# Kernel tuning notes

Measured on AMD Instinct MI355X. Metric: run time of the kernel, lower is better.

The kernel has to match this reference:

```python
import jax, jax.numpy as jnp
import numpy as np
from jax import lax


def _lstm_seq(x, W, U, b):
    """Keras-style LSTM over full sequence. x: [B,T,D] -> hs: [B,T,H].
    Gate order i, f, c(g), o; zero initial state; sigmoid/tanh activations."""
    B, T, D = x.shape
    H = U.shape[0]
    # Precompute input projection for all timesteps (one big GEMM).
    xz = jnp.einsum('btd,dg->btg', x, W) + b  # [B,T,4H]

    def step(carry, xz_t):
        h, c = carry
        z = xz_t + h @ U  # [B,4H]
        i, f, g, o = jnp.split(z, 4, axis=-1)
        i = jax.nn.sigmoid(i)
        f = jax.nn.sigmoid(f)
        g = jnp.tanh(g)
        o = jax.nn.sigmoid(o)
        c = f * c + i * g
        h = o * jnp.tanh(c)
        return (h, c), h

    h0 = jnp.zeros((B, H), dtype=x.dtype)
    c0 = jnp.zeros((B, H), dtype=x.dtype)
    (_, _), hs = lax.scan(step, (h0, c0), jnp.swapaxes(xz, 0, 1))  # hs: [T,B,H]
    return jnp.swapaxes(hs, 0, 1)  # [B,T,H]


def setup_inputs() -> dict:
    key = jax.random.key(0)
    ks = jax.random.split(key, 7)
    B, T, D, H = 64, 256, 1024, 1024
    s = 0.05  # weight scale to keep gates out of saturation
    x = jax.random.normal(ks[0], (B, T, 1, D), dtype=jnp.float32)
    Wf = jax.random.normal(ks[1], (D, 4 * H), dtype=jnp.float32) * s
    Uf = jax.random.normal(ks[2], (H, 4 * H), dtype=jnp.float32) * s
    bf = jnp.zeros((4 * H,), dtype=jnp.float32)
    Wb = jax.random.normal(ks[3], (D, 4 * H), dtype=jnp.float32) * s
    Ub = jax.random.normal(ks[4], (H, 4 * H), dtype=jnp.float32) * s
    bb = jnp.zeros((4 * H,), dtype=jnp.float32)
    return {"x": x, "Wf": Wf, "Uf": Uf, "bf": bf, "Wb": Wb, "Ub": Ub, "bb": bb}


def reference(x, Wf, Uf, bf, Wb, Ub, bb):
    # call(): squeeze axis=2, BiLSTM (concat), flatten. training=False -> dropout off.
    xs = jnp.squeeze(x, axis=2)  # [B,T,D]
    h_fwd = _lstm_seq(xs, Wf, Uf, bf)  # [B,T,H]
    # go_backwards=True: process reversed sequence; Bidirectional re-reverses output.
    h_bwd = _lstm_seq(xs[:, ::-1, :], Wb, Ub, bb)[:, ::-1, :]  # [B,T,H]
    out = jnp.concatenate([h_fwd, h_bwd], axis=-1)  # [B,T,2H]
    B = out.shape[0]
    return out.reshape(B, -1)  # Flatten -> [B, T*2H]
```

## Files before the change

### kernel.cpp

```cpp
#include <hip/hip_runtime.h>
#include <hip/hip_bf16.h>

typedef unsigned short u16;
typedef unsigned long long u64;
typedef short short8 __attribute__((ext_vector_type(8)));
typedef float floatx4 __attribute__((ext_vector_type(4)));

#define BATCH 64
#define SEQT  256
#define DDIM  1024
#define HDIM  1024
#define GDIM  4096
#define MROWS 16384

__device__ __forceinline__ u16 f2bf(float f) {
  unsigned u = __builtin_bit_cast(unsigned, f);
  u += 0x7fffu + ((u >> 16) & 1u);
  return (u16)(u >> 16);
}
__device__ __forceinline__ float bf2f(u16 v) {
  unsigned u = ((unsigned)v) << 16;
  return __builtin_bit_cast(float, u);
}
__device__ __forceinline__ float xz2f(float v) { return v; }
__device__ __forceinline__ float xz2f(u16 v) { return bf2f(v); }

template <typename T> __device__ __forceinline__ T f2xz(float v);
template <> __device__ __forceinline__ float f2xz<float>(float v) { return v; }
template <> __device__ __forceinline__ u16 f2xz<u16>(float v) { return f2bf(v); }

__device__ __forceinline__ float sigm(float x) { return 1.0f / (1.0f + __expf(-x)); }
__device__ __forceinline__ float tanh_(float x) {
  float a = __expf(2.0f * fabsf(x));
  float r = 1.0f - 2.0f / (a + 1.0f);
  return x >= 0.0f ? r : -r;
}

__device__ __forceinline__ void async16(const void* g, void* l) {
  __builtin_amdgcn_global_load_lds(
      (const __attribute__((address_space(1))) unsigned int*)g,
      (__attribute__((address_space(3))) unsigned int*)l, 16, 0, 0);
}

__device__ __forceinline__ void st_agent(unsigned* p, unsigned v) {
  __hip_atomic_store(p, v, __ATOMIC_RELAXED, __HIP_MEMORY_SCOPE_AGENT);
}

__device__ __forceinline__ void grid_barrier(unsigned* arrv, int wd, int l, unsigned epoch) {
  __syncthreads();
  if (threadIdx.x == 0)
    __hip_atomic_store(arrv + wd, epoch, __ATOMIC_RELAXED, __HIP_MEMORY_SCOPE_AGENT);
  if (threadIdx.x < 64) {
    unsigned a, b;
    do {
      __builtin_amdgcn_s_sleep(2);
      a = __hip_atomic_load(arrv + l,      __ATOMIC_RELAXED, __HIP_MEMORY_SCOPE_AGENT);
      b = __hip_atomic_load(arrv + 64 + l, __ATOMIC_RELAXED, __HIP_MEMORY_SCOPE_AGENT);
    } while (!__all(a >= epoch && b >= epoch));
  }
  __syncthreads();
}

__global__ __launch_bounds__(256) void k_cvt_x(const float* __restrict__ in,
                                               u16* __restrict__ out) {
  long i = ((long)blockIdx.x * 256 + threadIdx.x) * 4;
  float4 v = *(const float4*)(in + i);
  u16 o0 = f2bf(v.x), o1 = f2bf(v.y), o2 = f2bf(v.z), o3 = f2bf(v.w);
  unsigned lo = (unsigned)o0 | ((unsigned)o1 << 16);
  unsigned hi = (unsigned)o2 | ((unsigned)o3 << 16);
  uint2 p; p.x = lo; p.y = hi;
  *(uint2*)(out + i) = p;
}

__global__ __launch_bounds__(256) void k_tc(const float* __restrict__ S0, const float* __restrict__ S1,
                                            const float* __restrict__ S2, const float* __restrict__ S3,
                                            u16* __restrict__ D0, u16* __restrict__ D1,
                                            u16* __restrict__ D2, u16* __restrict__ D3) {
  const float* src; u16* dst;
  switch (blockIdx.z) {
    case 0: src = S0; dst = D0; break;
    case 1: src = S1; dst = D1; break;
    case 2: src = S2; dst = D2; break;
    default: src = S3; dst = D3; break;
  }
  __shared__ __align__(16) float tl[64][65];
  const int k0 = blockIdx.x * 64, n0 = blockIdx.y * 64;
  const int tid = threadIdx.x, col = tid & 63, rq = tid >> 6;
#pragma unroll
  for (int i = 0; i < 16; i++) {
    int r = i * 4 + rq;
    tl[r][col] = src[(long)(k0 + r) * GDIM + n0 + col];
  }
  __syncthreads();
#pragma unroll
  for (int i = 0; i < 16; i++) {
    int r = i * 4 + rq;
    dst[(long)(n0 + r) * DDIM + k0 + col] = f2bf(tl[col][r]);
  }
}

template <typename XZT>
__global__ __launch_bounds__(256) void k_gemm(const u16* __restrict__ A,
                                              const u16* __restrict__ BtF, const u16* __restrict__ BtB,
                                              const float* __restrict__ biasF, const float* __restrict__ biasB,
                                              XZT* __restrict__ xzF, XZT* __restrict__ xzB) {
  const u16* Bt = blockIdx.z ? BtB : BtF;
  const float* bias = blockIdx.z ? biasB : biasF;
  XZT* xz = blockIdx.z ? xzB : xzF;
  const int m0 = blockIdx.x * 128, n0 = blockIdx.y * 128;
  __shared__ __align__(16) u16 Al[128 * 32];
  __shared__ __align__(16) u16 Bl[128 * 32];
  const int tid = threadIdx.x, w = tid >> 6, l = tid & 63;
  const int wm = w & 1, wn = w >> 1;
  floatx4 acc[4][4];
#pragma unroll
  for (int i = 0; i < 4; i++)
#pragma unroll
    for (int j = 0; j < 4; j++) acc[i][j] = (floatx4)(0.0f);

  const int srow = w * 32 + (l >> 2);
  const char* Ag = (const char*)(A + (long)(m0 + srow) * DDIM) + (l & 3) * 16;
  const char* Bg = (const char*)(Bt + (long)(n0 + srow) * DDIM) + (l & 3) * 16;
  char* Asl = (char*)Al + w * 2048;
  char* Bsl = (char*)Bl + w * 2048;

  for (int kt = 0; kt < 32; kt++) {
    __syncthreads();
    async16(Ag, Asl);
    async16(Ag + 16 * 2048, Asl + 1024);
    async16(Bg, Bsl);
    async16(Bg + 16 * 2048, Bsl + 1024);
    Ag += 64; Bg += 64;
    __syncthreads();
    short8 af[4], bfr[4];
#pragma unroll
    for (int i = 0; i < 4; i++) {
      af[i]  = *(const short8*)(Al + (wm * 64 + i * 16 + (l & 15)) * 32 + (l >> 4) * 8);
      bfr[i] = *(const short8*)(Bl + (wn * 64 + i * 16 + (l & 15)) * 32 + (l >> 4) * 8);
    }
#pragma unroll
    for (int i = 0; i < 4; i++)
#pragma unroll
      for (int j = 0; j < 4; j++)
        acc[i][j] = __builtin_amdgcn_mfma_f32_16x16x32_bf16(af[i], bfr[j], acc[i][j], 0, 0, 0);
  }
  const int c = l & 15, q = l >> 4;
#pragma unroll
  for (int j = 0; j < 4; j++) {
    const int n = n0 + wn * 64 + j * 16 + c;
    const float bv = bias[n];
#pragma unroll
    for (int i = 0; i < 4; i++) {
      const long mb = (long)(m0 + wm * 64 + i * 16 + q * 4);
#pragma unroll
      for (int r = 0; r < 4; r++)
        xz[(mb + r) * GDIM + n] = f2xz<XZT>(acc[i][j][r] + bv);
    }
  }
}

template <typename XZT>
__global__ __launch_bounds__(256, 1) void k_lstm(const XZT* __restrict__ xzF, const XZT* __restrict__ xzB,
                                                 const u16* __restrict__ UtF, const u16* __restrict__ UtB,
                                                 u16* __restrict__ hbuf, float* __restrict__ out,
                                                 unsigned* __restrict__ bar) {
  const int wg = blockIdx.x;
  const int dir = wg >> 7;
  const int wd = wg & 127;
  const int j0 = wd * 8;
  const int tid = threadIdx.x;
  const int wave = tid >> 6, l = tid & 63;
  const int c = l & 15, q = l >> 4;
  const u16* Ut = dir ? UtB : UtF;
  const XZT* xz = dir ? xzB : xzF;
  unsigned* arrv = bar + dir * 128;
  u16* hb = hbuf + (long)dir * (2 * BATCH * HDIM);

  __shared__ __align__(16) u16 U1[16 * 1032];
  __shared__ float zl[64][33];

#pragma unroll
  for (int u8 = 0; u8 < 8; u8++) {
    int unit = u8 * 256 + tid;
    int r = unit >> 7, kc = unit & 127;
    int zr = (r < 8) ? (2048 + j0 + r) : (3072 + j0 + (r - 8));
    short8 v = *(const short8*)(Ut + (long)zr * DDIM + kc * 8);
    *(short8*)(&U1[r * 1032 + kc * 8]) = v;
  }
  const int zr0 = (c < 8) ? (j0 + c) : (1024 + j0 + (c - 8));
  const int zr1 = zr0 + 2048;
  short8 bU0[32];
#pragma unroll
  for (int kt = 0; kt < 32; kt++)
    bU0[kt] = *(const short8*)(Ut + (long)zr0 * DDIM + kt * 32 + q * 8);

  const int eb = tid >> 2;
  const int jj = (tid & 3) * 2;
  st_agent((unsigned*)(hb + eb * HDIM + j0 + jj), 0u);
  float cs0 = 0.0f, cs1 = 0.0f;

  const unsigned hvoff = (unsigned)(((wave * 16 + c) * HDIM + q * 8) * 2);

  float xv0[4], xv1[4];
  auto prefetch = [&](int s) {
    const int t = dir ? (SEQT - 1 - s) : s;
#pragma unroll
    for (int r = 0; r < 4; r++) {
      const long row = ((long)(wave * 16 + q * 4 + r) * SEQT + t) * GDIM;
      xv0[r] = xz2f(xz[row + zr0]);
      xv1[r] = xz2f(xz[row + zr1]);
    }
  };
  prefetch(0);

  for (int s = 0; s < SEQT; s++) {
    grid_barrier(arrv, wd, l, (unsigned)(s + 1));
    const int p = s & 1;
    const int t = dir ? (SEQT - 1 - s) : s;

    const u64 sbase = (u64)(hb + (long)p * (BATCH * HDIM));
    short8 hv[32];
#pragma unroll
    for (int kt = 0; kt < 32; kt++)
      asm volatile("global_load_dwordx4 %0, %1, %2 offset:%3 sc0 sc1"
                   : "=v"(hv[kt])
                   : "v"(hvoff), "s"(sbase), "n"(kt * 64));

    floatx4 a0 = (floatx4)(0.0f), a1 = (floatx4)(0.0f);
#pragma unroll
    for (int kt = 0; kt < 32; kt++) {
      asm volatile("s_waitcnt vmcnt(%1)" : "+v"(hv[kt]) : "n"(31 - kt));
      short8 b1 = *(const short8*)(&U1[c * 1032 + kt * 32 + q * 8]);
      a0 = __builtin_amdgcn_mfma_f32_16x16x32_bf16(hv[kt], bU0[kt], a0, 0, 0, 0);
      a1 = __builtin_amdgcn_mfma_f32_16x16x32_bf16(hv[kt], b1, a1, 0, 0, 0);
    }
#pragma unroll
    for (int r = 0; r < 4; r++) {
      const int m = wave * 16 + q * 4 + r;
      zl[m][c]      = a0[r] + xv0[r];
      zl[m][16 + c] = a1[r] + xv1[r];
    }
    __syncthreads();

    float zi0 = zl[eb][jj],      zi1 = zl[eb][jj + 1];
    float zf0 = zl[eb][8 + jj],  zf1 = zl[eb][8 + jj + 1];
    float zg0 = zl[eb][16 + jj], zg1 = zl[eb][16 + jj + 1];
    float zo0 = zl[eb][24 + jj], zo1 = zl[eb][24 + jj + 1];
    float i0 = sigm(zi0), f0 = sigm(zf0), g0 = tanh_(zg0), o0 = sigm(zo0);
    float i1 = sigm(zi1), f1 = sigm(zf1), g1 = tanh_(zg1), o1 = sigm(zo1);
    cs0 = f0 * cs0 + i0 * g0;
    cs1 = f1 * cs1 + i1 * g1;
    float h0v = o0 * tanh_(cs0), h1v = o1 * tanh_(cs1);

    unsigned hpair = (unsigned)f2bf(h0v) | ((unsigned)f2bf(h1v) << 16);
    st_agent((unsigned*)(hb + (long)(1 - p) * (BATCH * HDIM) + eb * HDIM + j0 + jj), hpair);
    float2 op = make_float2(h0v, h1v);
    *(float2*)(out + (long)eb * (SEQT * 2 * HDIM) + (long)t * (2 * HDIM) + dir * HDIM + j0 + jj) = op;

    if (s + 1 < SEQT) prefetch(s + 1);
  }
}

extern "C" void kernel_launch(void* const* d_in, const int* in_sizes, int n_in,
                              void* d_out, int out_size, void* d_ws, size_t ws_size,
                              hipStream_t stream) {
  const float* x   = (const float*)d_in[0];
  const float* Wf  = (const float*)d_in[1];
  const float* Uf  = (const float*)d_in[2];
  const float* bf_ = (const float*)d_in[3];
  const float* Wb  = (const float*)d_in[4];
  const float* Ub  = (const float*)d_in[5];
  const float* bb  = (const float*)d_in[6];
  float* out = (float*)d_out;
  char* ws = (char*)d_ws;

  const size_t SZ_XBF = (size_t)MROWS * DDIM * 2;
  const size_t SZ_WT  = (size_t)GDIM * DDIM * 2;
  const size_t SZ_H   = (size_t)2 * 2 * BATCH * HDIM * 2;

  size_t off = 2048;
  u16* xbf = (u16*)(ws + off); off += SZ_XBF;
  u16* WtF = (u16*)(ws + off); off += SZ_WT;
  u16* WtB = (u16*)(ws + off); off += SZ_WT;
  u16* UtF = (u16*)(ws + off); off += SZ_WT;
  u16* UtB = (u16*)(ws + off); off += SZ_WT;
  u16* hb  = (u16*)(ws + off); off += SZ_H;
  size_t xz_off = (off + 1023) & ~(size_t)1023;

  const size_t XZ_F32 = (size_t)MROWS * GDIM * 4;
  const size_t XZ_BF  = (size_t)MROWS * GDIM * 2;
  const bool fp32xz = ws_size >= xz_off + 2 * XZ_F32;

  unsigned* bar = (unsigned*)ws;
  hipMemsetAsync(bar, 0, 2048, stream);
  k_cvt_x<<<MROWS * DDIM / 1024, 256, 0, stream>>>(x, xbf);
  k_tc<<<dim3(16, 64, 4), 256, 0, stream>>>(Wf, Uf, Wb, Ub, WtF, UtF, WtB, UtB);

  if (fp32xz) {
    float* xzF = (float*)(ws + xz_off);
    float* xzB = (float*)(ws + xz_off + XZ_F32);
    k_gemm<float><<<dim3(128, 32, 2), 256, 0, stream>>>(xbf, WtF, WtB, bf_, bb, xzF, xzB);
    k_lstm<float><<<256, 256, 0, stream>>>(xzF, xzB, UtF, UtB, hb, out, bar);
  } else {
    u16* xzF = (u16*)(ws + xz_off);
    u16* xzB = (u16*)(ws + xz_off + XZ_BF);
    k_gemm<u16><<<dim3(128, 32, 2), 256, 0, stream>>>(xbf, WtF, WtB, bf_, bb, xzF, xzB);
    k_lstm<u16><<<256, 256, 0, stream>>>(xzF, xzB, UtF, UtB, hb, out, bar);
  }
}
```

Before: 3.535 ms.

## Mirror hidden state into per-XCD buffers so reads hit local L2

Each workgroup reads its XCD id from a hardware register and counts the workgroups per XCD and direction. Up to four leaders per group copy the shared h buffer each step into a per-XCD mirror and signal a flag. All workgroups then read h from the mirror with cached loads instead of system-coherent sc0 sc1 loads. The aim is to cut cross-XCD coherent traffic on the 64x1024 hidden state read every timestep, at the cost of an extra copy, an extra flag wait per step, and cache invalidations.

Result: no change. 3.604 ms (+1.9%).

```diff
diff --git a/kernel.cpp b/kernel.cpp
--- a/kernel.cpp
+++ b/kernel.cpp
@@ -12,6 +12,7 @@
 #define HDIM  1024
 #define GDIM  4096
 #define MROWS 16384
+#define NXCD  8
 
 __device__ __forceinline__ u16 f2bf(float f) {
   unsigned u = __builtin_bit_cast(unsigned, f);
@@ -44,6 +45,9 @@
 
 __device__ __forceinline__ void st_agent(unsigned* p, unsigned v) {
   __hip_atomic_store(p, v, __ATOMIC_RELAXED, __HIP_MEMORY_SCOPE_AGENT);
+}
+__device__ __forceinline__ unsigned ld_agent(const unsigned* p) {
+  return __hip_atomic_load(p, __ATOMIC_RELAXED, __HIP_MEMORY_SCOPE_AGENT);
 }
 
 __device__ __forceinline__ void grid_barrier(unsigned* arrv, int wd, int l, unsigned epoch) {
@@ -162,7 +166,8 @@
 template <typename XZT>
 __global__ __launch_bounds__(256, 1) void k_lstm(const XZT* __restrict__ xzF, const XZT* __restrict__ xzB,
                                                  const u16* __restrict__ UtF, const u16* __restrict__ UtB,
-                                                 u16* __restrict__ hbuf, float* __restrict__ out,
+                                                 u16* __restrict__ hbuf, u16* __restrict__ mirror,
+                                                 float* __restrict__ out,
                                                  unsigned* __restrict__ bar) {
   const int wg = blockIdx.x;
   const int dir = wg >> 7;
@@ -173,11 +178,26 @@
   const int c = l & 15, q = l >> 4;
   const u16* Ut = dir ? UtB : UtF;
   const XZT* xz = dir ? xzB : xzF;
-  unsigned* arrv = bar + dir * 128;
+  unsigned* arrv  = bar + dir * 128;
+  unsigned* flags = bar + 256;
+  unsigned* cnti  = bar + 512;
+  unsigned* cany  = bar + 768;
   u16* hb = hbuf + (long)dir * (2 * BATCH * HDIM);
 
   __shared__ __align__(16) u16 U1[16 * 1032];
   __shared__ float zl[64][33];
+  __shared__ unsigned s_xcd, s_old, s_nl, s_use;
+
+  if (tid == 0) {
+    unsigned xcc;
+    asm volatile("s_getreg_b32 %0, hwreg(20, 0, 32)" : "=s"(xcc));
+    xcc &= 7;
+    s_xcd = xcc;
+    const unsigned g = xcc * 2 + (unsigned)dir;
+    s_old = atomicAdd(&cnti[g], 1u);
+    if (s_old == 0)
+      *(volatile unsigned*)&cany[g * 32] = 0xC0FFEE00u | g;
+  }
 
 #pragma unroll
   for (int u8 = 0; u8 < 8; u8++) {
@@ -194,12 +214,20 @@
   for (int kt = 0; kt < 32; kt++)
     bU0[kt] = *(const short8*)(Ut + (long)zr0 * DDIM + kt * 32 + q * 8);
 
+  __syncthreads();
+  const unsigned myx = s_xcd;
+  const unsigned lidx = s_old;
+  const unsigned grp = myx * 2 + (unsigned)dir;
+  u16* mirb = mirror + (size_t)grp * (BATCH * HDIM);
+  unsigned* flg = flags + grp * 16;
+
   const int eb = tid >> 2;
   const int jj = (tid & 3) * 2;
   st_agent((unsigned*)(hb + eb * HDIM + j0 + jj), 0u);
   float cs0 = 0.0f, cs1 = 0.0f;
 
   const unsigned hvoff = (unsigned)(((wave * 16 + c) * HDIM + q * 8) * 2);
+  const unsigned cpoff = (unsigned)(wave * 8192 + l * 16);
 
   float xv0[4], xv1[4];
   auto prefetch = [&](int s) {
@@ -213,18 +241,64 @@
   };
   prefetch(0);
 
+  unsigned nl = 4, use_mir = 0;
   for (int s = 0; s < SEQT; s++) {
     grid_barrier(arrv, wd, l, (unsigned)(s + 1));
+    if (s == 0) {
+      asm volatile("buffer_inv sc0" ::: "memory");
+      if (tid == 0) {
+        unsigned gsz = ld_agent(&cnti[grp]);
+        s_nl = gsz < 4 ? gsz : 4;
+        s_use = (*(volatile unsigned*)&cany[grp * 32] == (0xC0FFEE00u | grp)) ? 1u : 0u;
+      }
+      __syncthreads();
+      nl = s_nl; use_mir = s_use;
+    }
     const int p = s & 1;
     const int t = dir ? (SEQT - 1 - s) : s;
-
     const u64 sbase = (u64)(hb + (long)p * (BATCH * HDIM));
+    const u64 mbase = (u64)mirb;
+
+    if (lidx < 4) {
+      for (unsigned ch = lidx; ch < 4; ch += nl) {
+        const unsigned cb = ch * 32768u + cpoff;
+        short8 cv[8];
+#pragma unroll
+        for (int i = 0; i < 8; i++)
+          asm volatile("global_load_dwordx4 %0, %1, %2 sc0 sc1"
+                       : "=v"(cv[i]) : "v"(cb + i * 1024u), "s"(sbase));
+#pragma unroll
+        for (int i = 0; i < 8; i++) {
+          asm volatile("s_waitcnt vmcnt(7)" : "+v"(cv[i]));
+          asm volatile("global_store_dwordx4 %0, %1, %2"
+                       :: "v"(cb + i * 1024u), "v"(cv[i]), "s"(mbase));
+        }
+      }
+      asm volatile("s_waitcnt vmcnt(0)" ::: "memory");
+      __syncthreads();
+      if (tid == 0) atomicAdd(flg, 1u);
+    }
+
     short8 hv[32];
-#pragma unroll
-    for (int kt = 0; kt < 32; kt++)
-      asm volatile("global_load_dwordx4 %0, %1, %2 offset:%3 sc0 sc1"
-                   : "=v"(hv[kt])
-                   : "v"(hvoff), "s"(sbase), "n"(kt * 64));
+    if (use_mir) {
+      if (tid == 0) {
+        const unsigned target = nl * (unsigned)(s + 1);
+        while (ld_agent(flg) < target) __builtin_amdgcn_s_sleep(1);
+      }
+      __syncthreads();
+      asm volatile("buffer_inv sc0" ::: "memory");
+#pragma unroll
+      for (int kt = 0; kt < 32; kt++)
+        asm volatile("global_load_dwordx4 %0, %1, %2 offset:%3"
+                     : "=v"(hv[kt])
+                     : "v"(hvoff), "s"(mbase), "n"(kt * 64));
+    } else {
+#pragma unroll
+      for (int kt = 0; kt < 32; kt++)
+        asm volatile("global_load_dwordx4 %0, %1, %2 offset:%3 sc0 sc1"
+                     : "=v"(hv[kt])
+                     : "v"(hvoff), "s"(sbase), "n"(kt * 64));
+    }
 
     floatx4 a0 = (floatx4)(0.0f), a1 = (floatx4)(0.0f);
 #pragma unroll
@@ -277,14 +351,16 @@
   const size_t SZ_XBF = (size_t)MROWS * DDIM * 2;
   const size_t SZ_WT  = (size_t)GDIM * DDIM * 2;
   const size_t SZ_H   = (size_t)2 * 2 * BATCH * HDIM * 2;
-
-  size_t off = 2048;
+  const size_t SZ_MIR = (size_t)NXCD * 2 * BATCH * HDIM * 2;
+
+  size_t off = 8192;
   u16* xbf = (u16*)(ws + off); off += SZ_XBF;
   u16* WtF = (u16*)(ws + off); off += SZ_WT;
   u16* WtB = (u16*)(ws + off); off += SZ_WT;
   u16* UtF = (u16*)(ws + off); off += SZ_WT;
   u16* UtB = (u16*)(ws + off); off += SZ_WT;
   u16* hb  = (u16*)(ws + off); off += SZ_H;
+  u16* mir = (u16*)(ws + off); off += SZ_MIR;
   size_t xz_off = (off + 1023) & ~(size_t)1023;
 
   const size_t XZ_F32 = (size_t)MROWS * GDIM * 4;
@@ -292,7 +368,7 @@
   const bool fp32xz = ws_size >= xz_off + 2 * XZ_F32;
 
   unsigned* bar = (unsigned*)ws;
-  hipMemsetAsync(bar, 0, 2048, stream);
+  hipMemsetAsync(bar, 0, 8192, stream);
   k_cvt_x<<<MROWS * DDIM / 1024, 256, 0, stream>>>(x, xbf);
   k_tc<<<dim3(16, 64, 4), 256, 0, stream>>>(Wf, Uf, Wb, Ub, WtF, UtF, WtB, UtB);
 
@@ -300,11 +376,11 @@
     float* xzF = (float*)(ws + xz_off);
     float* xzB = (float*)(ws + xz_off + XZ_F32);
     k_gemm<float><<<dim3(128, 32, 2), 256, 0, stream>>>(xbf, WtF, WtB, bf_, bb, xzF, xzB);
-    k_lstm<float><<<256, 256, 0, stream>>>(xzF, xzB, UtF, UtB, hb, out, bar);
+    k_lstm<float><<<256, 256, 0, stream>>>(xzF, xzB, UtF, UtB, hb, mir, out, bar);
   } else {
     u16* xzF = (u16*)(ws + xz_off);
     u16* xzB = (u16*)(ws + xz_off + XZ_BF);
     k_gemm<u16><<<dim3(128, 32, 2), 256, 0, stream>>>(xbf, WtF, WtB, bf_, bb, xzF, xzB);
-    k_lstm<u16><<<256, 256, 0, stream>>>(xzF, xzB, UtF, UtB, hb, out, bar);
-  }
-}
+    k_lstm<u16><<<256, 256, 0, stream>>>(xzF, xzB, UtF, UtB, hb, mir, out, bar);
+  }
+}
```
